# Performance work log

Hardware: AMD Instinct MI355X
Metric: run time of the kernel (lower is better)

The kernel has to match this reference:

```python
import jax, jax.numpy as jnp
import numpy as np

N = 100000
E = 1600000
IN = 128
HID = 32
HEADS = 4
HID2 = 8  # hidden_channels / 4
OUT = 1


def setup_inputs() -> dict:
    key = jax.random.key(0)
    ks = jax.random.split(key, 13)
    def glorot(k, shape):
        fan = sum(shape[-2:]) if len(shape) >= 2 else shape[-1]
        return jax.random.normal(k, shape, dtype=jnp.float32) * (2.0 / fan) ** 0.5
    return {
        "x": jax.random.normal(ks[0], (N, IN), dtype=jnp.float32),
        "edge_index": jax.random.randint(ks[1], (2, E), 0, N, dtype=jnp.int32),
        "edge_attr": jax.random.normal(ks[2], (E, 8), dtype=jnp.float32),  # ignored by GATConv (edge_dim=None)
        "W1": glorot(ks[3], (IN, HEADS * HID)),
        "a_src1": glorot(ks[4], (HEADS, HID)),
        "a_dst1": glorot(ks[5], (HEADS, HID)),
        "b1": jnp.zeros((HEADS * HID,), dtype=jnp.float32),
        "W2": glorot(ks[6], (HEADS * HID, 1 * HID2)),
        "a_src2": glorot(ks[7], (1, HID2)),
        "a_dst2": glorot(ks[8], (1, HID2)),
        "b2": jnp.zeros((HID2,), dtype=jnp.float32),
        "Wlin": glorot(ks[9], (HID2, OUT)),
        "blin": jnp.zeros((OUT,), dtype=jnp.float32),
    }


def gat_layer(x, W, a_src, a_dst, bias, src, dst, num_nodes, concat):
    """PyG GATConv (edge_dim=None): gather -> LeakyReLU attn -> segment softmax over dst -> scatter-add."""
    H, C = a_src.shape
    h = (x @ W).reshape(num_nodes, H, C)                        # [N, H, C]
    alpha_s = jnp.einsum('nhc,hc->nh', h, a_src)                # [N, H]
    alpha_d = jnp.einsum('nhc,hc->nh', h, a_dst)
    e = jax.nn.leaky_relu(alpha_s[src] + alpha_d[dst], 0.2)     # [E, H]
    m = jax.ops.segment_max(e, dst, num_segments=num_nodes)     # softmax over incoming edges per dst
    ex = jnp.exp(e - m[dst])
    denom = jax.ops.segment_sum(ex, dst, num_segments=num_nodes)
    alpha = ex / (denom[dst] + 1e-16)                           # [E, H]
    out = jax.ops.segment_sum(h[src] * alpha[:, :, None], dst, num_segments=num_nodes)  # [N, H, C]
    out = out.reshape(num_nodes, H * C) if concat else out.mean(axis=1)
    return out + bias


def reference(x, edge_index, edge_attr, W1, a_src1, a_dst1, b1, W2, a_src2, a_dst2, b2, Wlin, blin):
    n = x.shape[0]
    loops = jnp.arange(n, dtype=edge_index.dtype)               # add_self_loops=True (PyG default)
    src = jnp.concatenate([edge_index[0], loops])
    dst = jnp.concatenate([edge_index[1], loops])
    h = jax.nn.elu(gat_layer(x, W1, a_src1, a_dst1, b1, src, dst, n, True))
    h = jax.nn.elu(gat_layer(h, W2, a_src2, a_dst2, b2, src, dst, n, False))
    return jax.nn.sigmoid(h @ Wlin + blin)                      # [N, 1]
```

## Files before the change

kernel.cpp:

```cpp
#include <hip/hip_runtime.h>
#include <hip/hip_bf16.h>

__device__ __forceinline__ float lrelu02(float v) { return v > 0.f ? v : 0.2f * v; }

__device__ __forceinline__ float bf2f(unsigned short u) {
    union { unsigned int i; float f; } v; v.i = ((unsigned int)u) << 16; return v.f;
}
__device__ __forceinline__ unsigned short f2bf(float f) {
    union { float f; unsigned int i; } v; v.f = f;
    unsigned int x = v.i;
    return (unsigned short)((x + 0x7fffu + ((x >> 16) & 1u)) >> 16);
}
__device__ __forceinline__ float blo(unsigned int u) {
    union { unsigned int i; float f; } v; v.i = u << 16; return v.f;
}
__device__ __forceinline__ float bhi(unsigned int u) {
    union { unsigned int i; float f; } v; v.i = u & 0xffff0000u; return v.f;
}

__global__ __launch_bounds__(256) void gemm1_k(
    const float* __restrict__ x, const float* __restrict__ W1,
    const float* __restrict__ aw_s, const float* __restrict__ aw_d,
    unsigned short* __restrict__ h1b, float* __restrict__ as1, float* __restrict__ ad1, int N,
    const int* __restrict__ ei, int E, int* __restrict__ deg, int* __restrict__ rank)
{
    {
        const int total = E + N;
        const int stride = gridDim.x * 256;
        for (int e = blockIdx.x * 256 + threadIdx.x; e < total; e += stride) {
            int d = (e < E) ? ei[E + e] : (e - E);
            rank[e] = atomicAdd(&deg[d], 1);
        }
    }

    __shared__ unsigned int Wl[128 * 64];
    {
        const float4* W4 = (const float4*)W1;
        for (int i = threadIdx.x; i < 128 * 32; i += 256) {
            float4 f = W4[i];
            unsigned int lo = f2bf(f.x) | ((unsigned)f2bf(f.y) << 16);
            unsigned int hi = f2bf(f.z) | ((unsigned)f2bf(f.w) << 16);
            int k = i >> 5, t = i & 31;
            Wl[k * 64 + 2 * t]     = lo;
            Wl[k * 64 + 2 * t + 1] = hi;
        }
    }

    const int cl = threadIdx.x & 15;
    const int rg = threadIdx.x >> 4;
    const int head = cl >> 2;
    const int row0 = blockIdx.x * 64 + rg * 4;
    __syncthreads();

    const float4* x4[4];
    bool rv[4];
    #pragma unroll
    for (int r = 0; r < 4; ++r) {
        int rr = row0 + r;
        rv[r] = rr < N;
        int rc = rv[r] ? rr : (N - 1);
        x4[r] = (const float4*)(x + (size_t)rc * 128);
    }

    float acc[4][8];
    #pragma unroll
    for (int r = 0; r < 4; ++r)
        #pragma unroll
        for (int c = 0; c < 8; ++c) acc[r][c] = 0.f;

    for (int k4 = 0; k4 < 32; ++k4) {
        float4 xv[4];
        #pragma unroll
        for (int r = 0; r < 4; ++r) xv[r] = x4[r][k4];
        #pragma unroll
        for (int kk = 0; kk < 4; ++kk) {
            const int k = k4 * 4 + kk;
            const uint4 wp = *(const uint4*)(Wl + k * 64 + cl * 4);
            const float w0 = blo(wp.x), w1 = bhi(wp.x);
            const float w2 = blo(wp.y), w3 = bhi(wp.y);
            const float w4 = blo(wp.z), w5 = bhi(wp.z);
            const float w6 = blo(wp.w), w7 = bhi(wp.w);
            #pragma unroll
            for (int r = 0; r < 4; ++r) {
                const float xk = kk == 0 ? xv[r].x : kk == 1 ? xv[r].y : kk == 2 ? xv[r].z : xv[r].w;
                acc[r][0] = fmaf(xk, w0, acc[r][0]);
                acc[r][1] = fmaf(xk, w1, acc[r][1]);
                acc[r][2] = fmaf(xk, w2, acc[r][2]);
                acc[r][3] = fmaf(xk, w3, acc[r][3]);
                acc[r][4] = fmaf(xk, w4, acc[r][4]);
                acc[r][5] = fmaf(xk, w5, acc[r][5]);
                acc[r][6] = fmaf(xk, w6, acc[r][6]);
                acc[r][7] = fmaf(xk, w7, acc[r][7]);
            }
        }
    }

    float ws_[8], wd_[8];
    #pragma unroll
    for (int c = 0; c < 8; ++c) { ws_[c] = aw_s[cl * 8 + c]; wd_[c] = aw_d[cl * 8 + c]; }

    #pragma unroll
    for (int r = 0; r < 4; ++r) {
        float s = 0.f, d = 0.f;
        #pragma unroll
        for (int c = 0; c < 8; ++c) { s = fmaf(acc[r][c], ws_[c], s); d = fmaf(acc[r][c], wd_[c], d); }
        s += __shfl_xor(s, 1); s += __shfl_xor(s, 2);
        d += __shfl_xor(d, 1); d += __shfl_xor(d, 2);
        if (rv[r]) {
            if ((cl & 3) == 0) { as1[(row0 + r) * 4 + head] = s; ad1[(row0 + r) * 4 + head] = d; }
            uint4 pk;
            pk.x = f2bf(acc[r][0]) | ((unsigned)f2bf(acc[r][1]) << 16);
            pk.y = f2bf(acc[r][2]) | ((unsigned)f2bf(acc[r][3]) << 16);
            pk.z = f2bf(acc[r][4]) | ((unsigned)f2bf(acc[r][5]) << 16);
            pk.w = f2bf(acc[r][6]) | ((unsigned)f2bf(acc[r][7]) << 16);
            *(uint4*)(h1b + (size_t)(row0 + r) * 128 + cl * 8) = pk;
        }
    }
}

__global__ __launch_bounds__(256) void blocksum_k(
    const int* __restrict__ deg, int N, int* __restrict__ bsum)
{
    __shared__ int sh[256];
    int i = blockIdx.x * 256 + threadIdx.x;
    sh[threadIdx.x] = (i < N) ? deg[i] : 0;
    __syncthreads();
    for (int off = 128; off; off >>= 1) {
        if (threadIdx.x < off) sh[threadIdx.x] += sh[threadIdx.x + off];
        __syncthreads();
    }
    if (threadIdx.x == 0) bsum[blockIdx.x] = sh[0];
}

__global__ __launch_bounds__(1024) void scanbsum_k(int* __restrict__ bsum, int nb)
{
    __shared__ int buf[1024];
    __shared__ int carry;
    if (threadIdx.x == 0) carry = 0;
    __syncthreads();
    for (int base = 0; base < nb; base += 1024) {
        int i = base + threadIdx.x;
        int v = (i < nb) ? bsum[i] : 0;
        buf[threadIdx.x] = v;
        __syncthreads();
        for (int off = 1; off < 1024; off <<= 1) {
            int t = (threadIdx.x >= off) ? buf[threadIdx.x - off] : 0;
            __syncthreads();
            buf[threadIdx.x] += t;
            __syncthreads();
        }
        if (i < nb) bsum[i] = buf[threadIdx.x] - v + carry;
        __syncthreads();
        if (threadIdx.x == 0) carry += buf[1023];
        __syncthreads();
    }
}

__global__ __launch_bounds__(256) void rowptr_k(
    const int* __restrict__ deg, const int* __restrict__ bsum, int N, int E,
    int* __restrict__ rowptr)
{
    __shared__ int buf[256];
    int i = blockIdx.x * 256 + threadIdx.x;
    int v = (i < N) ? deg[i] : 0;
    buf[threadIdx.x] = v;
    __syncthreads();
    for (int off = 1; off < 256; off <<= 1) {
        int t = (threadIdx.x >= off) ? buf[threadIdx.x - off] : 0;
        __syncthreads();
        buf[threadIdx.x] += t;
        __syncthreads();
    }
    if (i < N) rowptr[i] = bsum[blockIdx.x] + buf[threadIdx.x] - v;
    if (i == 0) rowptr[N] = E + N;
}

__global__ __launch_bounds__(256) void place_k(
    const int* __restrict__ ei, int E, int N,
    const int* __restrict__ rank, const int* __restrict__ rowptr,
    int* __restrict__ csr)
{
    int e = blockIdx.x * 256 + threadIdx.x;
    if (e >= E + N) return;
    int s, d;
    if (e < E) { s = ei[e]; d = ei[E + e]; } else { s = d = e - E; }
    csr[rowptr[d] + rank[e]] = s;
}

__global__ __launch_bounds__(256) void gat1_k(
    const int* __restrict__ csr, const int* __restrict__ rowptr,
    const float* __restrict__ as1, const float* __restrict__ ad1,
    const unsigned short* __restrict__ h1b, const float* __restrict__ b1,
    const float* __restrict__ W2, const float* __restrict__ aw_s2, const float* __restrict__ aw_d2,
    float* __restrict__ g, float* __restrict__ as2, float* __restrict__ ad2, int N)
{
    __shared__ float red[4][8][12];
    const int wv   = threadIdx.x >> 6;
    const int wid  = (blockIdx.x * 256 + threadIdx.x) >> 6;
    const int lane = threadIdx.x & 63;
    if (wid >= N) return;
    const int start = rowptr[wid], end = rowptr[wid + 1];
    const int i16 = lane & 15;
    const int hh  = lane >> 4;
    const float adh = ad1[wid * 4 + hh];
    const float mh  = lrelu02(as1[wid * 4 + hh] + adh);
    const unsigned short* hb = h1b + lane * 2;

    float den = 0.f, acc0 = 0.f, acc1 = 0.f;
    int k0 = start;
    for (; k0 + 16 <= end; k0 += 16) {
        int s = csr[k0 + i16];
        float w = __expf(lrelu02(as1[s * 4 + hh] + adh) - mh);
        den += w;
        #pragma unroll
        for (int e = 0; e < 16; ++e) {
            int se = __builtin_amdgcn_readlane(s, e);
            float we = __shfl(w, e, 16);
            unsigned int pv = *(const unsigned int*)(hb + (size_t)se * 128);
            acc0 = fmaf(bf2f((unsigned short)pv), we, acc0);
            acc1 = fmaf(bf2f((unsigned short)(pv >> 16)), we, acc1);
        }
    }
    int cnt = end - k0;
    if (cnt > 0) {
        int s = (i16 < cnt) ? csr[k0 + i16] : wid;
        float w = (i16 < cnt) ? __expf(lrelu02(as1[s * 4 + hh] + adh) - mh) : 0.f;
        den += w;
        for (int e = 0; e < cnt; ++e) {
            int se = __builtin_amdgcn_readlane(s, e);
            float we = __shfl(w, e, 16);
            unsigned int pv = *(const unsigned int*)(hb + (size_t)se * 128);
            acc0 = fmaf(bf2f((unsigned short)pv), we, acc0);
            acc1 = fmaf(bf2f((unsigned short)(pv >> 16)), we, acc1);
        }
    }
    den += __shfl_xor(den, 1); den += __shfl_xor(den, 2);
    den += __shfl_xor(den, 4); den += __shfl_xor(den, 8);
    const float rden = 1.f / (den + 1e-16f);
    float v0 = acc0 * rden + b1[lane * 2];
    float v1 = acc1 * rden + b1[lane * 2 + 1];
    v0 = v0 > 0.f ? v0 : expm1f(v0);
    v1 = v1 > 0.f ? v1 : expm1f(v1);

    const float4 a0 = *(const float4*)(W2 + 16 * lane);
    const float4 a1 = *(const float4*)(W2 + 16 * lane + 4);
    const float4 b0 = *(const float4*)(W2 + 16 * lane + 8);
    const float4 b1v = *(const float4*)(W2 + 16 * lane + 12);
    float p[8];
    p[0] = v0 * a0.x + v1 * b0.x;  p[1] = v0 * a0.y + v1 * b0.y;
    p[2] = v0 * a0.z + v1 * b0.z;  p[3] = v0 * a0.w + v1 * b0.w;
    p[4] = v0 * a1.x + v1 * b1v.x; p[5] = v0 * a1.y + v1 * b1v.y;
    p[6] = v0 * a1.z + v1 * b1v.z; p[7] = v0 * a1.w + v1 * b1v.w;
    #pragma unroll
    for (int j = 0; j < 8; ++j) {
        p[j] += __shfl_xor(p[j], 8);
        p[j] += __shfl_xor(p[j], 16);
        p[j] += __shfl_xor(p[j], 32);
    }
    if (lane < 8) {
        #pragma unroll
        for (int j = 0; j < 8; ++j) red[wv][lane][j] = p[j];
    }
    if (lane < 8) {
        float gj = 0.f;
        #pragma unroll
        for (int c = 0; c < 8; ++c) gj += red[wv][c][lane];
        g[(size_t)wid * 8 + lane] = gj;
        float ts = gj * aw_s2[lane], td = gj * aw_d2[lane];
        ts += __shfl_xor(ts, 1); ts += __shfl_xor(ts, 2); ts += __shfl_xor(ts, 4);
        td += __shfl_xor(td, 1); td += __shfl_xor(td, 2); td += __shfl_xor(td, 4);
        if (lane == 0) { as2[wid] = ts; ad2[wid] = td; }
    }
}

__global__ __launch_bounds__(256) void gat2_k(
    const int* __restrict__ csr, const int* __restrict__ rowptr,
    const float* __restrict__ as2, const float* __restrict__ ad2,
    const float* __restrict__ g, const float* __restrict__ b2_,
    const float* __restrict__ Wlin, const float* __restrict__ blin,
    float* __restrict__ out, int N)
{
    const int wid  = (blockIdx.x * 256 + threadIdx.x) >> 6;
    const int lane = threadIdx.x & 63;
    if (wid >= N) return;
    const int start = rowptr[wid], end = rowptr[wid + 1];
    const int i8  = lane & 7;
    const int grp = lane >> 3;
    const float adh = ad2[wid];
    const float mh  = lrelu02(as2[wid] + adh);
    float den = 0.f, acc = 0.f;
    int k0 = start;
    for (; k0 + 8 <= end; k0 += 8) {
        int s = csr[k0 + i8];
        float w = __expf(lrelu02(as2[s] + adh) - mh);
        den += w;
        int   se = __shfl(s, grp, 8);
        float we = __shfl(w, grp, 8);
        acc = fmaf(we, g[(size_t)se * 8 + i8], acc);
    }
    int cnt = end - k0;
    if (cnt > 0) {
        int s = (i8 < cnt) ? csr[k0 + i8] : wid;
        float w = (i8 < cnt) ? __expf(lrelu02(as2[s] + adh) - mh) : 0.f;
        den += w;
        int   se = __shfl(s, grp, 8);
        float we = __shfl(w, grp, 8);
        acc = fmaf(we, g[(size_t)se * 8 + i8], acc);
    }
    den += __shfl_xor(den, 1); den += __shfl_xor(den, 2); den += __shfl_xor(den, 4);
    acc += __shfl_xor(acc, 8); acc += __shfl_xor(acc, 16); acc += __shfl_xor(acc, 32);
    float v = acc / (den + 1e-16f) + b2_[i8];
    v = v > 0.f ? v : expm1f(v);
    float t = v * Wlin[i8];
    t += __shfl_xor(t, 1); t += __shfl_xor(t, 2); t += __shfl_xor(t, 4);
    if (lane == 0) out[wid] = 1.f / (1.f + __expf(-(t + blin[0])));
}

extern "C" void kernel_launch(void* const* d_in, const int* in_sizes, int n_in,
                              void* d_out, int out_size, void* d_ws, size_t ws_size,
                              hipStream_t stream)
{
    (void)n_in; (void)out_size; (void)ws_size;
    const float* x    = (const float*)d_in[0];
    const int*   ei   = (const int*)d_in[1];
    const float* W1   = (const float*)d_in[3];
    const float* as1w = (const float*)d_in[4];
    const float* ad1w = (const float*)d_in[5];
    const float* b1   = (const float*)d_in[6];
    const float* W2   = (const float*)d_in[7];
    const float* as2w = (const float*)d_in[8];
    const float* ad2w = (const float*)d_in[9];
    const float* b2v  = (const float*)d_in[10];
    const float* Wlin = (const float*)d_in[11];
    const float* blin = (const float*)d_in[12];

    const int N = in_sizes[0] / 128;
    const int E = in_sizes[1] / 2;
    const int total = E + N;

    float* p = (float*)d_ws;
    unsigned short* h1b = (unsigned short*)p; p += (size_t)N * 64;
    float* as1  = p; p += (size_t)N * 4;
    float* ad1  = p; p += (size_t)N * 4;
    float* g    = p; p += (size_t)N * 8;
    float* as2  = p; p += (size_t)N;
    float* ad2  = p; p += (size_t)N;
    int* deg    = (int*)p; p += (size_t)N;
    int* rowptr = (int*)p; p += (size_t)N + 1;
    int* bsum   = (int*)p; p += ((size_t)N + 255) / 256;
    int* rank   = (int*)p; p += (size_t)total;
    int* csr    = (int*)p; p += (size_t)total;

    const int eb = (total + 255) / 256;
    const int nb = (N + 255) / 256;

    hipMemsetAsync(deg, 0, (size_t)N * sizeof(int), stream);
    gemm1_k<<<(N + 63) / 64, 256, 0, stream>>>(x, W1, as1w, ad1w, h1b, as1, ad1, N,
                                               ei, E, deg, rank);
    blocksum_k<<<nb, 256, 0, stream>>>(deg, N, bsum);
    scanbsum_k<<<1, 1024, 0, stream>>>(bsum, nb);
    rowptr_k<<<nb, 256, 0, stream>>>(deg, bsum, N, E, rowptr);
    place_k<<<eb, 256, 0, stream>>>(ei, E, N, rank, rowptr, csr);

    gat1_k<<<(N * 64 + 255) / 256, 256, 0, stream>>>(csr, rowptr, as1, ad1, h1b, b1,
                                                     W2, as2w, ad2w, g, as2, ad2, N);
    gat2_k<<<(N * 64 + 255) / 256, 256, 0, stream>>>(csr, rowptr, as2, ad2, g, b2v, Wlin, blin,
                                                     (float*)d_out, N);
}
```

Before: 440.3 us.

## Use bf16 MFMA with split-precision x for first-layer GEMM

```diff
diff --git a/kernel.cpp b/kernel.cpp
--- a/kernel.cpp
+++ b/kernel.cpp
@@ -18,7 +18,10 @@
     union { unsigned int i; float f; } v; v.i = u & 0xffff0000u; return v.f;
 }
 
-__global__ __launch_bounds__(256) void gemm1_k(
+typedef float f32x4 __attribute__((ext_vector_type(4)));
+typedef short s16x8 __attribute__((ext_vector_type(8)));
+
+__global__ __launch_bounds__(512) void gemm1_k(
     const float* __restrict__ x, const float* __restrict__ W1,
     const float* __restrict__ aw_s, const float* __restrict__ aw_d,
     unsigned short* __restrict__ h1b, float* __restrict__ as1, float* __restrict__ ad1, int N,
@@ -26,94 +29,99 @@
 {
     {
         const int total = E + N;
-        const int stride = gridDim.x * 256;
-        for (int e = blockIdx.x * 256 + threadIdx.x; e < total; e += stride) {
+        const int stride = gridDim.x * 512;
+        for (int e = blockIdx.x * 512 + threadIdx.x; e < total; e += stride) {
             int d = (e < E) ? ei[E + e] : (e - E);
             rank[e] = atomicAdd(&deg[d], 1);
         }
     }
 
-    __shared__ unsigned int Wl[128 * 64];
+    __shared__ unsigned short Wt[128 * 128];
     {
         const float4* W4 = (const float4*)W1;
-        for (int i = threadIdx.x; i < 128 * 32; i += 256) {
+        for (int i = threadIdx.x; i < 128 * 32; i += 512) {
             float4 f = W4[i];
-            unsigned int lo = f2bf(f.x) | ((unsigned)f2bf(f.y) << 16);
-            unsigned int hi = f2bf(f.z) | ((unsigned)f2bf(f.w) << 16);
-            int k = i >> 5, t = i & 31;
-            Wl[k * 64 + 2 * t]     = lo;
-            Wl[k * 64 + 2 * t + 1] = hi;
-        }
-    }
-
-    const int cl = threadIdx.x & 15;
-    const int rg = threadIdx.x >> 4;
-    const int head = cl >> 2;
-    const int row0 = blockIdx.x * 64 + rg * 4;
+            int k = i >> 5, c4 = (i & 31) * 4;
+            #pragma unroll
+            for (int j = 0; j < 4; ++j) {
+                int col = c4 + j;
+                float fv = j == 0 ? f.x : j == 1 ? f.y : j == 2 ? f.z : f.w;
+                Wt[col * 128 + (k ^ ((col & 7) << 3))] = f2bf(fv);
+            }
+        }
+    }
+
+    const int lane = threadIdx.x & 63;
+    const int wv   = threadIdx.x >> 6;
+    const int li   = lane & 15;
+    const int kg   = lane >> 2 >> 2;
+    const int row0 = blockIdx.x * 128 + wv * 16;
+
+    const int rc = (row0 + li < N) ? (row0 + li) : (N - 1);
+    const float4* xr = (const float4*)(x + (size_t)rc * 128);
+
+    f32x4 acc[8];
+    #pragma unroll
+    for (int ct = 0; ct < 8; ++ct) acc[ct] = {0.f, 0.f, 0.f, 0.f};
+
     __syncthreads();
 
-    const float4* x4[4];
-    bool rv[4];
-    #pragma unroll
-    for (int r = 0; r < 4; ++r) {
-        int rr = row0 + r;
-        rv[r] = rr < N;
-        int rc = rv[r] ? rr : (N - 1);
-        x4[r] = (const float4*)(x + (size_t)rc * 128);
-    }
-
-    float acc[4][8];
-    #pragma unroll
-    for (int r = 0; r < 4; ++r)
-        #pragma unroll
-        for (int c = 0; c < 8; ++c) acc[r][c] = 0.f;
-
-    for (int k4 = 0; k4 < 32; ++k4) {
-        float4 xv[4];
-        #pragma unroll
-        for (int r = 0; r < 4; ++r) xv[r] = x4[r][k4];
-        #pragma unroll
-        for (int kk = 0; kk < 4; ++kk) {
-            const int k = k4 * 4 + kk;
-            const uint4 wp = *(const uint4*)(Wl + k * 64 + cl * 4);
-            const float w0 = blo(wp.x), w1 = bhi(wp.x);
-            const float w2 = blo(wp.y), w3 = bhi(wp.y);
-            const float w4 = blo(wp.z), w5 = bhi(wp.z);
-            const float w6 = blo(wp.w), w7 = bhi(wp.w);
+    #pragma unroll
+    for (int ks = 0; ks < 4; ++ks) {
+        float4 f0 = xr[ks * 8 + kg * 2];
+        float4 f1 = xr[ks * 8 + kg * 2 + 1];
+        float xf[8] = {f0.x, f0.y, f0.z, f0.w, f1.x, f1.y, f1.z, f1.w};
+        s16x8 ahi, alo;
+        #pragma unroll
+        for (int j = 0; j < 8; ++j) {
+            unsigned short h = f2bf(xf[j]);
+            ahi[j] = (short)h;
+            alo[j] = (short)f2bf(xf[j] - bf2f(h));
+        }
+        const int kbase = ks * 32 + kg * 8;
+        #pragma unroll
+        for (int ct = 0; ct < 8; ++ct) {
+            const int col = ct * 16 + li;
+            const s16x8 b = *reinterpret_cast<const s16x8*>(
+                Wt + col * 128 + (kbase ^ ((col & 7) << 3)));
+            acc[ct] = __builtin_amdgcn_mfma_f32_16x16x32_bf16(ahi, b, acc[ct], 0, 0, 0);
+            acc[ct] = __builtin_amdgcn_mfma_f32_16x16x32_bf16(alo, b, acc[ct], 0, 0, 0);
+        }
+    }
+
+    float aws_[8], awd_[8];
+    #pragma unroll
+    for (int t = 0; t < 8; ++t) { aws_[t] = aw_s[t * 16 + li]; awd_[t] = aw_d[t * 16 + li]; }
+
+    #pragma unroll
+    for (int i = 0; i < 4; ++i) {
+        const int gr = row0 + (lane >> 4) * 4 + i;
+        const bool valid = gr < N;
+        float s0 = acc[0][i] * aws_[0] + acc[1][i] * aws_[1];
+        float s1 = acc[2][i] * aws_[2] + acc[3][i] * aws_[3];
+        float s2 = acc[4][i] * aws_[4] + acc[5][i] * aws_[5];
+        float s3 = acc[6][i] * aws_[6] + acc[7][i] * aws_[7];
+        float d0 = acc[0][i] * awd_[0] + acc[1][i] * awd_[1];
+        float d1 = acc[2][i] * awd_[2] + acc[3][i] * awd_[3];
+        float d2 = acc[4][i] * awd_[4] + acc[5][i] * awd_[5];
+        float d3 = acc[6][i] * awd_[6] + acc[7][i] * awd_[7];
+        #pragma unroll
+        for (int m = 1; m < 16; m <<= 1) {
+            s0 += __shfl_xor(s0, m, 16); s1 += __shfl_xor(s1, m, 16);
+            s2 += __shfl_xor(s2, m, 16); s3 += __shfl_xor(s3, m, 16);
+            d0 += __shfl_xor(d0, m, 16); d1 += __shfl_xor(d1, m, 16);
+            d2 += __shfl_xor(d2, m, 16); d3 += __shfl_xor(d3, m, 16);
+        }
+        if (valid) {
+            if (li < 4) {
+                float sv = li == 0 ? s0 : li == 1 ? s1 : li == 2 ? s2 : s3;
+                float dv = li == 0 ? d0 : li == 1 ? d1 : li == 2 ? d2 : d3;
+                as1[gr * 4 + li] = sv;
+                ad1[gr * 4 + li] = dv;
+            }
             #pragma unroll
-            for (int r = 0; r < 4; ++r) {
-                const float xk = kk == 0 ? xv[r].x : kk == 1 ? xv[r].y : kk == 2 ? xv[r].z : xv[r].w;
-                acc[r][0] = fmaf(xk, w0, acc[r][0]);
-                acc[r][1] = fmaf(xk, w1, acc[r][1]);
-                acc[r][2] = fmaf(xk, w2, acc[r][2]);
-                acc[r][3] = fmaf(xk, w3, acc[r][3]);
-                acc[r][4] = fmaf(xk, w4, acc[r][4]);
-                acc[r][5] = fmaf(xk, w5, acc[r][5]);
-                acc[r][6] = fmaf(xk, w6, acc[r][6]);
-                acc[r][7] = fmaf(xk, w7, acc[r][7]);
-            }
-        }
-    }
-
-    float ws_[8], wd_[8];
-    #pragma unroll
-    for (int c = 0; c < 8; ++c) { ws_[c] = aw_s[cl * 8 + c]; wd_[c] = aw_d[cl * 8 + c]; }
-
-    #pragma unroll
-    for (int r = 0; r < 4; ++r) {
-        float s = 0.f, d = 0.f;
-        #pragma unroll
-        for (int c = 0; c < 8; ++c) { s = fmaf(acc[r][c], ws_[c], s); d = fmaf(acc[r][c], wd_[c], d); }
-        s += __shfl_xor(s, 1); s += __shfl_xor(s, 2);
-        d += __shfl_xor(d, 1); d += __shfl_xor(d, 2);
-        if (rv[r]) {
-            if ((cl & 3) == 0) { as1[(row0 + r) * 4 + head] = s; ad1[(row0 + r) * 4 + head] = d; }
-            uint4 pk;
-            pk.x = f2bf(acc[r][0]) | ((unsigned)f2bf(acc[r][1]) << 16);
-            pk.y = f2bf(acc[r][2]) | ((unsigned)f2bf(acc[r][3]) << 16);
-            pk.z = f2bf(acc[r][4]) | ((unsigned)f2bf(acc[r][5]) << 16);
-            pk.w = f2bf(acc[r][6]) | ((unsigned)f2bf(acc[r][7]) << 16);
-            *(uint4*)(h1b + (size_t)(row0 + r) * 128 + cl * 8) = pk;
+            for (int ct = 0; ct < 8; ++ct)
+                h1b[(size_t)gr * 128 + ct * 16 + li] = f2bf(acc[ct][i]);
         }
     }
 }
@@ -355,8 +363,8 @@
     const int nb = (N + 255) / 256;
 
     hipMemsetAsync(deg, 0, (size_t)N * sizeof(int), stream);
-    gemm1_k<<<(N + 63) / 64, 256, 0, stream>>>(x, W1, as1w, ad1w, h1b, as1, ad1, N,
-                                               ei, E, deg, rank);
+    gemm1_k<<<(N + 127) / 128, 512, 0, stream>>>(x, W1, as1w, ad1w, h1b, as1, ad1, N,
+                                                 ei, E, deg, rank);
     blocksum_k<<<nb, 256, 0, stream>>>(deg, N, bsum);
     scanbsum_k<<<1, 1024, 0, stream>>>(bsum, nb);
     rowptr_k<<<nb, 256, 0, stream>>>(deg, bsum, N, E, rowptr);
```

Measured after the change: 427.6 us. 1.03x faster.
